# Optimization experiments

Measured on AMD Instinct MI355X. Metric: run time of the kernel, lower is better.

Reference implementation:

```python
import jax, jax.numpy as jnp
import numpy as np

N_NODES = 65536
IN_CH = 512
HIDDEN = 256          # hidden_channels[0] == encoder_hidden
OUT_CH = 8
NUM_GRAPHS = 32
MAX_LEN = 4096        # static pad bound (>= max per-graph length)
BN_EPS = 1e-5


def _make_batch_ids():
    # deterministic ragged per-graph lengths summing exactly to N_NODES
    rng = np.random.RandomState(0)
    d = rng.randint(-512, 512, size=NUM_GRAPHS)
    d[-1] -= d.sum()
    lengths = N_NODES // NUM_GRAPHS + d          # each in ~[1536, 2560] <= MAX_LEN
    return jnp.asarray(np.repeat(np.arange(NUM_GRAPHS), lengths), dtype=jnp.int32)


def setup_inputs() -> dict:
    key = jax.random.key(0)
    ks = jax.random.split(key, 12)
    f32 = jnp.float32
    inp = {
        'x_res': jax.random.normal(ks[0], (N_NODES, IN_CH), dtype=f32),
        'batch': _make_batch_ids(),
        # BatchNorm1d affine params
        'bn_gamma': jnp.ones((IN_CH,), f32),
        'bn_beta': jnp.zeros((IN_CH,), f32),
        # input2transformer: Linear(C,2H) GELU Linear(2H,H) GELU Linear(H,H)
        'W1': jax.random.normal(ks[1], (IN_CH, 2 * HIDDEN), f32) * (1.0 / np.sqrt(IN_CH)),
        'b1': jnp.zeros((2 * HIDDEN,), f32),
        'W2': jax.random.normal(ks[2], (2 * HIDDEN, HIDDEN), f32) * (1.0 / np.sqrt(2 * HIDDEN)),
        'b2': jnp.zeros((HIDDEN,), f32),
        'W3': jax.random.normal(ks[3], (HIDDEN, HIDDEN), f32) * (1.0 / np.sqrt(HIDDEN)),
        'b3': jnp.zeros((HIDDEN,), f32),
        # out_angles: Linear(encoder_hidden, out_ch) GELU DynamicTanh Tanh
        'Wo': jax.random.normal(ks[4], (HIDDEN, OUT_CH), f32) * (1.0 / np.sqrt(HIDDEN)),
        'bo': jnp.zeros((OUT_CH,), f32),
        'dyt_alpha': jnp.asarray(0.5, f32),
        'dyt_w': jnp.ones((OUT_CH,), f32),
        'dyt_b': jnp.zeros((OUT_CH,), f32),
    }
    return inp


def _forward(x_res, batch, bn_gamma, bn_beta, W1, b1, W2, b2, W3, b3,
             Wo, bo, dyt_alpha, dyt_w, dyt_b):
    # BatchNorm1d (training-mode batch stats, biased var), dropout is identity (eval)
    mu = jnp.mean(x_res, axis=0)
    var = jnp.mean((x_res - mu) ** 2, axis=0)
    x = (x_res - mu) * jax.lax.rsqrt(var + BN_EPS) * bn_gamma + bn_beta
    # input2transformer MLP (torch GELU default = exact erf)
    gelu = lambda t: jax.nn.gelu(t, approximate=False)
    x = gelu(x @ W1 + b1)
    x = gelu(x @ W2 + b2)
    x = x @ W3 + b3                                   # [N, HIDDEN]
    # ragged -> padded: scatter each node into (graph, position-in-graph)
    counts = jax.ops.segment_sum(jnp.ones_like(batch, dtype=jnp.int32), batch,
                                 num_segments=NUM_GRAPHS)
    offsets = jnp.concatenate([jnp.zeros((1,), jnp.int32),
                               jnp.cumsum(counts)[:-1].astype(jnp.int32)])
    pos = jnp.arange(N_NODES, dtype=jnp.int32) - offsets[batch]
    x_pad = jnp.zeros((NUM_GRAPHS, MAX_LEN, HIDDEN), x.dtype).at[batch, pos].set(x)
    z = jnp.transpose(x_pad, (1, 0, 2))               # [MAX_LEN, NUM_GRAPHS, HIDDEN] (stack dim=1)
    # out_angles head: Linear -> GELU -> DynamicTanh -> Tanh
    a = gelu(z @ Wo + bo)
    a = dyt_w * jnp.tanh(dyt_alpha * a) + dyt_b       # DynamicTanh (channels_last)
    return jnp.tanh(a)                                # [MAX_LEN, NUM_GRAPHS, OUT_CH]


def reference(x_res, batch, bn_gamma, bn_beta, W1, b1, W2, b2, W3, b3,
              Wo, bo, dyt_alpha, dyt_w, dyt_b):
    return _forward(x_res, batch, bn_gamma, bn_beta, W1, b1, W2, b2, W3, b3,
                    Wo, bo, dyt_alpha, dyt_w, dyt_b)
```

## Files before the change

### kernel.cpp

```cpp
#include <hip/hip_runtime.h>
#include <hip/hip_bf16.h>

#define N_NODES 65536
#define IN_CH 512
#define HIDDEN 256
#define OUT_CH 8
#define NUM_GRAPHS 32
#define MAX_LEN 4096
#define BN_EPS 1e-5f
#define BN_BLOCKS 2048

using short8  = __attribute__((ext_vector_type(8))) short;
using floatx4 = __attribute__((ext_vector_type(4))) float;
typedef unsigned int u32;
typedef unsigned short u16;

__device__ inline u16 f2b(float f) {
    u32 u = __float_as_uint(f);
    u += 0x7FFFu + ((u >> 16) & 1u);
    return (u16)(u >> 16);
}
__device__ inline float gelu_f(float x) {
    float z = x + 0.044715f * x * x * x;
    float e = __builtin_exp2f(-2.3022078f * z);
    return x * __builtin_amdgcn_rcpf(1.0f + e);
}
__device__ inline float tanh_f(float y) {
    y = fminf(fmaxf(y, -20.0f), 20.0f);
    float t = __builtin_exp2f(2.885390082f * y);
    return (t - 1.0f) * __builtin_amdgcn_rcpf(t + 1.0f);
}
__device__ inline void load_lds16(const void* g, void* l) {
    __builtin_amdgcn_global_load_lds(
        (const __attribute__((address_space(1))) u32*)g,
        (__attribute__((address_space(3))) u32*)l, 16, 0, 0);
}

__global__ __launch_bounds__(256) void statscast_k(const float* __restrict__ x,
                                                   u16* __restrict__ xb,
                                                   float4* __restrict__ partials) {
    __shared__ float4 sS[128];
    __shared__ float4 sQ[128];
    int tid = threadIdx.x;
    int half = tid >> 7;
    int c = tid & 127;
    const float4* x4 = (const float4*)x;
    uint2* xb2 = (uint2*)xb;
    float4 s = make_float4(0.f, 0.f, 0.f, 0.f);
    float4 q = make_float4(0.f, 0.f, 0.f, 0.f);
    int row0 = blockIdx.x * 32;
#pragma unroll
    for (int r = half; r < 32; r += 2) {
        size_t off = (size_t)(row0 + r) * 128 + c;
        float4 v = x4[off];
        s.x += v.x; s.y += v.y; s.z += v.z; s.w += v.w;
        q.x += v.x * v.x; q.y += v.y * v.y; q.z += v.z * v.z; q.w += v.w * v.w;
        uint2 o;
        o.x = (u32)f2b(v.x) | ((u32)f2b(v.y) << 16);
        o.y = (u32)f2b(v.z) | ((u32)f2b(v.w) << 16);
        xb2[off] = o;
    }
    if (half == 1) { sS[c] = s; sQ[c] = q; }
    __syncthreads();
    if (half == 0) {
        float4 s2 = sS[c], q2 = sQ[c];
        s.x += s2.x; s.y += s2.y; s.z += s2.z; s.w += s2.w;
        q.x += q2.x; q.y += q2.y; q.z += q2.z; q.w += q2.w;
        partials[(size_t)blockIdx.x * 256 + c * 2]     = make_float4(s.x, q.x, s.y, q.y);
        partials[(size_t)blockIdx.x * 256 + c * 2 + 1] = make_float4(s.z, q.z, s.w, q.w);
    }
}

__global__ __launch_bounds__(256) void bn_reduce_k(const float4* __restrict__ partials,
                                                   const float* __restrict__ gamma,
                                                   const float* __restrict__ beta,
                                                   float* __restrict__ scale,
                                                   float* __restrict__ shift) {
    __shared__ float4 sd[256];
    int tid = threadIdx.x;
    int g = blockIdx.x;
    float4 a = make_float4(0.f, 0.f, 0.f, 0.f);
    for (int r = tid; r < BN_BLOCKS; r += 256) {
        float4 v = partials[(size_t)r * 256 + g];
        a.x += v.x; a.y += v.y; a.z += v.z; a.w += v.w;
    }
    sd[tid] = a;
    __syncthreads();
    for (int st = 128; st > 0; st >>= 1) {
        if (tid < st) {
            float4 b = sd[tid + st];
            float4 m = sd[tid];
            m.x += b.x; m.y += b.y; m.z += b.z; m.w += b.w;
            sd[tid] = m;
        }
        __syncthreads();
    }
    if (tid == 0) {
        float4 t = sd[0];
        int c0 = g * 2, c1 = g * 2 + 1;
        const float inv = 1.0f / N_NODES;
        float mu0 = t.x * inv, var0 = t.y * inv - mu0 * mu0;
        float mu1 = t.z * inv, var1 = t.w * inv - mu1 * mu1;
        float sc0 = gamma[c0] * rsqrtf(var0 + BN_EPS);
        float sc1 = gamma[c1] * rsqrtf(var1 + BN_EPS);
        scale[c0] = sc0; shift[c0] = beta[c0] - mu0 * sc0;
        scale[c1] = sc1; shift[c1] = beta[c1] - mu1 * sc1;
    }
}

__global__ __launch_bounds__(256) void prep_k(const float* __restrict__ W1,
                                              const float* __restrict__ W2,
                                              const float* __restrict__ W3,
                                              const float* __restrict__ b1,
                                              const float* __restrict__ scale,
                                              const float* __restrict__ shift,
                                              u16* __restrict__ W1T,
                                              u16* __restrict__ W2T,
                                              u16* __restrict__ W3T,
                                              float* __restrict__ b1f,
                                              const int* __restrict__ batch,
                                              int* __restrict__ offsets) {
    int bid = blockIdx.x;
    int tid = threadIdx.x;
    if (bid < 1792) {
        int idx = bid * 256 + tid;
        if (idx < 262144) {
            int k = idx >> 9, m = idx & 511;
            W1T[(size_t)m * 512 + k] = f2b(scale[k] * W1[idx]);
        } else if (idx < 262144 + 131072) {
            int i = idx - 262144;
            int k = i >> 8, m = i & 255;
            W2T[(size_t)m * 512 + k] = f2b(W2[i]);
        } else {
            int i = idx - 393216;
            int k = i >> 8, m = i & 255;
            W3T[(size_t)m * 256 + k] = f2b(W3[i]);
        }
        if (bid == 0 && tid < NUM_GRAPHS + 1) {
            int gph = tid;
            int lo = 0, hi = N_NODES;
            while (lo < hi) {
                int mid = (lo + hi) >> 1;
                if (batch[mid] < gph) lo = mid + 1; else hi = mid;
            }
            offsets[gph] = lo;
        }
    } else {
        int m = (bid - 1792) * 256 + tid;
        float acc = b1[m];
#pragma unroll 16
        for (int k = 0; k < 512; ++k) acc += shift[k] * W1[k * 512 + m];
        b1f[m] = acc;
    }
}

template <int DO_GELU, int NXB>
__global__ __launch_bounds__(512) void gemm_bt_k(const u16* __restrict__ A,
                                                 const u16* __restrict__ BT,
                                                 const float* __restrict__ bias,
                                                 u16* __restrict__ C,
                                                 int K, int M) {
    __shared__ __align__(16) u16 As[256 * 64];
    __shared__ __align__(16) u16 Bs[128 * 64];
    int tid = threadIdx.x;
    int lane = tid & 63;
    int bid = blockIdx.x;
    int xcd = bid & 7;
    int slot = bid >> 3;
    int rloc = slot / NXB;
    int colb = slot - rloc * NXB;
    int row0 = (xcd * 32 + rloc) * 256;
    int col0 = colb * 128;
    int wave = tid >> 6;
    int wr = (wave >> 1) * 64;
    int wc = (wave & 1) * 64;
    int l15 = lane & 15;
    int q = lane >> 4;

    floatx4 acc[4][4] = {};

    const int nkt = K >> 6;
    for (int kt = 0; kt < nkt; ++kt) {
        int k0 = kt << 6;
#pragma unroll
        for (int s = 0; s < 4; ++s) {
            int li = s * 512 + tid;
            int r = li >> 3;
            int g = li & 7;
            int gs = g ^ (r & 7);
            load_lds16(&A[(size_t)(row0 + r) * K + k0 + gs * 8], &As[li * 8]);
        }
#pragma unroll
        for (int s = 0; s < 2; ++s) {
            int li = s * 512 + tid;
            int r = li >> 3;
            int g = li & 7;
            int gs = g ^ (r & 7);
            load_lds16(&BT[(size_t)(col0 + r) * K + k0 + gs * 8], &Bs[li * 8]);
        }
        __syncthreads();
#pragma unroll
        for (int ks = 0; ks < 2; ++ks) {
            int gidx = ks * 4 + q;
            short8 af[4], bg[4];
#pragma unroll
            for (int i = 0; i < 4; ++i) {
                int row = wr + i * 16 + l15;
                af[i] = *(const short8*)&As[row * 64 + (gidx ^ (row & 7)) * 8];
            }
#pragma unroll
            for (int j = 0; j < 4; ++j) {
                int row = wc + j * 16 + l15;
                bg[j] = *(const short8*)&Bs[row * 64 + (gidx ^ (row & 7)) * 8];
            }
#pragma unroll
            for (int i = 0; i < 4; ++i)
#pragma unroll
                for (int j = 0; j < 4; ++j)
                    acc[i][j] = __builtin_amdgcn_mfma_f32_16x16x32_bf16(bg[j], af[i], acc[i][j], 0, 0, 0);
        }
        __syncthreads();
    }
#pragma unroll
    for (int i = 0; i < 4; ++i) {
        size_t rbase = (size_t)(row0 + wr + i * 16 + l15) * M;
#pragma unroll
        for (int j = 0; j < 4; ++j) {
            int c = col0 + wc + j * 16 + q * 4;
            float4 b4 = *(const float4*)&bias[c];
            float v0 = acc[i][j][0] + b4.x;
            float v1 = acc[i][j][1] + b4.y;
            float v2 = acc[i][j][2] + b4.z;
            float v3 = acc[i][j][3] + b4.w;
            if (DO_GELU) { v0 = gelu_f(v0); v1 = gelu_f(v1); v2 = gelu_f(v2); v3 = gelu_f(v3); }
            uint2 pk;
            pk.x = (u32)f2b(v0) | ((u32)f2b(v1) << 16);
            pk.y = (u32)f2b(v2) | ((u32)f2b(v3) << 16);
            *(uint2*)&C[rbase + c] = pk;
        }
    }
}

__global__ __launch_bounds__(256) void head_k(const u16* __restrict__ h3,
                                              const float* __restrict__ Wo,
                                              const float* __restrict__ bo,
                                              const int* __restrict__ offsets,
                                              const float* __restrict__ alpha_p,
                                              const float* __restrict__ dyt_w,
                                              const float* __restrict__ dyt_b,
                                              float* __restrict__ out) {
    __shared__ float sWo[HIDDEN * OUT_CH];
    __shared__ int soff[NUM_GRAPHS + 1];
    int tid = threadIdx.x;
#pragma unroll
    for (int i = 0; i < 8; ++i) sWo[i * 256 + tid] = Wo[i * 256 + tid];
    if (tid < NUM_GRAPHS + 1) soff[tid] = offsets[tid];
    __syncthreads();
    int idx = blockIdx.x * 256 + tid;
    int g = idx & 31;
    int p = idx >> 5;
    int n = soff[g] + p;
    bool valid = n < soff[g + 1];
    float acc[8];
#pragma unroll
    for (int c = 0; c < 8; ++c) acc[c] = bo[c];
    if (valid) {
        const uint4* hr = (const uint4*)(h3 + (size_t)n * HIDDEN);
#pragma unroll 4
        for (int kk = 0; kk < 32; ++kk) {
            uint4 v = hr[kk];
            u32 u[4] = {v.x, v.y, v.z, v.w};
#pragma unroll
            for (int pp = 0; pp < 4; ++pp) {
                float h0 = __uint_as_float(u[pp] << 16);
                float h1 = __uint_as_float(u[pp] & 0xFFFF0000u);
                const float* w0 = &sWo[(kk * 8 + pp * 2) * 8];
                const float* w1 = w0 + 8;
#pragma unroll
                for (int c = 0; c < 8; ++c) acc[c] += h0 * w0[c];
#pragma unroll
                for (int c = 0; c < 8; ++c) acc[c] += h1 * w1[c];
            }
        }
    }
    float alpha = alpha_p[0];
    float res[8];
#pragma unroll
    for (int c = 0; c < 8; ++c) {
        float a = gelu_f(acc[c]);
        a = dyt_w[c] * tanh_f(alpha * a) + dyt_b[c];
        res[c] = tanh_f(a);
    }
    float4* o = (float4*)(out + (size_t)idx * OUT_CH);
    o[0] = make_float4(res[0], res[1], res[2], res[3]);
    o[1] = make_float4(res[4], res[5], res[6], res[7]);
}

extern "C" void kernel_launch(void* const* d_in, const int* in_sizes, int n_in,
                              void* d_out, int out_size, void* d_ws, size_t ws_size,
                              hipStream_t stream) {
    (void)in_sizes; (void)n_in; (void)out_size; (void)ws_size;
    const float* x_res = (const float*)d_in[0];
    const int*   batch = (const int*)d_in[1];
    const float* gamma = (const float*)d_in[2];
    const float* beta  = (const float*)d_in[3];
    const float* W1    = (const float*)d_in[4];
    const float* b1    = (const float*)d_in[5];
    const float* W2    = (const float*)d_in[6];
    const float* b2    = (const float*)d_in[7];
    const float* W3    = (const float*)d_in[8];
    const float* b3    = (const float*)d_in[9];
    const float* Wo    = (const float*)d_in[10];
    const float* bo    = (const float*)d_in[11];
    const float* alpha = (const float*)d_in[12];
    const float* dyt_w = (const float*)d_in[13];
    const float* dyt_b = (const float*)d_in[14];
    float* out = (float*)d_out;

    char* ws = (char*)d_ws;
    float* scale = (float*)(ws + 0);
    float* shift = (float*)(ws + 2048);
    float* b1f   = (float*)(ws + 4096);
    int*   offs  = (int*)(ws + 8192);
    u16* W1T = (u16*)(ws + 16384);
    u16* W2T = (u16*)(ws + 16384 + 524288);
    u16* W3T = (u16*)(ws + 16384 + 524288 + 262144);
    const size_t MB = 1024 * 1024;
    u16* xb = (u16*)(ws + 2 * MB);
    u16* h1 = (u16*)(ws + 66 * MB);
    u16* h2 = (u16*)(ws + 2 * MB);
    u16* h3 = (u16*)(ws + 66 * MB);
    float4* partials = (float4*)(ws + 66 * MB);

    statscast_k<<<BN_BLOCKS, 256, 0, stream>>>(x_res, xb, partials);
    bn_reduce_k<<<256, 256, 0, stream>>>(partials, gamma, beta, scale, shift);
    prep_k<<<1794, 256, 0, stream>>>(W1, W2, W3, b1, scale, shift,
                                     W1T, W2T, W3T, b1f, batch, offs);
    gemm_bt_k<1, 4><<<1024, 512, 0, stream>>>(xb, W1T, b1f, h1, 512, 512);
    gemm_bt_k<1, 2><<<512, 512, 0, stream>>>(h1, W2T, b2, h2, 512, 256);
    gemm_bt_k<0, 2><<<512, 512, 0, stream>>>(h2, W3T, b3, h3, 256, 256);
    head_k<<<512, 256, 0, stream>>>(h3, Wo, bo, offs, alpha, dyt_w, dyt_b, out);
}
```

Before: 375.6 us.

## Fuse second and third MLP GEMMs into one kernel keeping h2 in LDS

Replaces the separate W2 and W3 GEMM launches with a single kernel. Each 64-row block computes h2 = GELU(h1·W2+b2), stores it swizzled in shared memory, then multiplies it by W3 to write h3. This removes the h2 global write and read and one launch. In exchange, weight fragments are read directly from global or L2 without LDS staging, and the first GEMM is specialized with compile-time K and M.

Measured after the change: 397.2 us. 5.8% more time.

```diff
diff --git a/kernel.cpp b/kernel.cpp
--- a/kernel.cpp
+++ b/kernel.cpp
@@ -154,12 +154,11 @@
     }
 }
 
-template <int DO_GELU, int NXB>
-__global__ __launch_bounds__(512) void gemm_bt_k(const u16* __restrict__ A,
-                                                 const u16* __restrict__ BT,
-                                                 const float* __restrict__ bias,
-                                                 u16* __restrict__ C,
-                                                 int K, int M) {
+__global__ __launch_bounds__(512) void gemm1_k(const u16* __restrict__ A,
+                                               const u16* __restrict__ BT,
+                                               const float* __restrict__ bias,
+                                               u16* __restrict__ C) {
+    const int K = 512, M = 512;
     __shared__ __align__(16) u16 As[256 * 64];
     __shared__ __align__(16) u16 Bs[128 * 64];
     int tid = threadIdx.x;
@@ -167,8 +166,8 @@
     int bid = blockIdx.x;
     int xcd = bid & 7;
     int slot = bid >> 3;
-    int rloc = slot / NXB;
-    int colb = slot - rloc * NXB;
+    int rloc = slot >> 2;
+    int colb = slot & 3;
     int row0 = (xcd * 32 + rloc) * 256;
     int col0 = colb * 128;
     int wave = tid >> 6;
@@ -179,8 +178,7 @@
 
     floatx4 acc[4][4] = {};
 
-    const int nkt = K >> 6;
-    for (int kt = 0; kt < nkt; ++kt) {
+    for (int kt = 0; kt < 8; ++kt) {
         int k0 = kt << 6;
 #pragma unroll
         for (int s = 0; s < 4; ++s) {
@@ -228,15 +226,126 @@
         for (int j = 0; j < 4; ++j) {
             int c = col0 + wc + j * 16 + q * 4;
             float4 b4 = *(const float4*)&bias[c];
-            float v0 = acc[i][j][0] + b4.x;
-            float v1 = acc[i][j][1] + b4.y;
-            float v2 = acc[i][j][2] + b4.z;
-            float v3 = acc[i][j][3] + b4.w;
-            if (DO_GELU) { v0 = gelu_f(v0); v1 = gelu_f(v1); v2 = gelu_f(v2); v3 = gelu_f(v3); }
+            float v0 = gelu_f(acc[i][j][0] + b4.x);
+            float v1 = gelu_f(acc[i][j][1] + b4.y);
+            float v2 = gelu_f(acc[i][j][2] + b4.z);
+            float v3 = gelu_f(acc[i][j][3] + b4.w);
             uint2 pk;
             pk.x = (u32)f2b(v0) | ((u32)f2b(v1) << 16);
             pk.y = (u32)f2b(v2) | ((u32)f2b(v3) << 16);
             *(uint2*)&C[rbase + c] = pk;
+        }
+    }
+}
+
+__global__ __launch_bounds__(256, 3) void mlp_tail_k(const u16* __restrict__ h1,
+                                                     const u16* __restrict__ W2T,
+                                                     const u16* __restrict__ W3T,
+                                                     const float* __restrict__ b2,
+                                                     const float* __restrict__ b3,
+                                                     u16* __restrict__ h3) {
+    __shared__ __align__(16) u16 As[64 * 64];
+    __shared__ __align__(16) u16 H2[64 * 256];
+    int tid = threadIdx.x;
+    int lane = tid & 63;
+    int w = tid >> 6;
+    int l15 = lane & 15;
+    int q = lane >> 4;
+    int row0 = blockIdx.x * 64;
+
+    {
+        floatx4 acc[4][4] = {};
+        for (int kt = 0; kt < 8; ++kt) {
+            int k0 = kt << 6;
+#pragma unroll
+            for (int s = 0; s < 2; ++s) {
+                int li = s * 256 + tid;
+                int r = li >> 3;
+                int g = li & 7;
+                int gs = g ^ (r & 7);
+                load_lds16(&h1[(size_t)(row0 + r) * 512 + k0 + gs * 8], &As[li * 8]);
+            }
+            __syncthreads();
+#pragma unroll
+            for (int ks = 0; ks < 2; ++ks) {
+                int gidx = ks * 4 + q;
+                short8 af[4], bg[4];
+#pragma unroll
+                for (int j = 0; j < 4; ++j)
+                    bg[j] = *(const short8*)&W2T[(size_t)(w * 64 + j * 16 + l15) * 512 + k0 + ks * 32 + q * 8];
+#pragma unroll
+                for (int i = 0; i < 4; ++i) {
+                    int row = i * 16 + l15;
+                    af[i] = *(const short8*)&As[row * 64 + (gidx ^ (row & 7)) * 8];
+                }
+#pragma unroll
+                for (int i = 0; i < 4; ++i)
+#pragma unroll
+                    for (int j = 0; j < 4; ++j)
+                        acc[i][j] = __builtin_amdgcn_mfma_f32_16x16x32_bf16(bg[j], af[i], acc[i][j], 0, 0, 0);
+            }
+            __syncthreads();
+        }
+#pragma unroll
+        for (int j = 0; j < 4; ++j) {
+            int cl = w * 64 + j * 16 + q * 4;
+            float4 b4 = *(const float4*)&b2[cl];
+            int gg = cl >> 3;
+            int half = (q & 1) * 4;
+#pragma unroll
+            for (int i = 0; i < 4; ++i) {
+                int row = i * 16 + l15;
+                int sg = (gg & ~7) | ((gg ^ row) & 7);
+                float v0 = gelu_f(acc[i][j][0] + b4.x);
+                float v1 = gelu_f(acc[i][j][1] + b4.y);
+                float v2 = gelu_f(acc[i][j][2] + b4.z);
+                float v3 = gelu_f(acc[i][j][3] + b4.w);
+                uint2 pk;
+                pk.x = (u32)f2b(v0) | ((u32)f2b(v1) << 16);
+                pk.y = (u32)f2b(v2) | ((u32)f2b(v3) << 16);
+                *(uint2*)&H2[row * 256 + sg * 8 + half] = pk;
+            }
+        }
+    }
+    __syncthreads();
+
+    {
+        floatx4 acc[4][4] = {};
+#pragma unroll
+        for (int ks = 0; ks < 8; ++ks) {
+            int g2 = ks * 4 + q;
+            short8 af[4], bg[4];
+#pragma unroll
+            for (int j = 0; j < 4; ++j)
+                bg[j] = *(const short8*)&W3T[(size_t)(w * 64 + j * 16 + l15) * 256 + ks * 32 + q * 8];
+#pragma unroll
+            for (int i = 0; i < 4; ++i) {
+                int row = i * 16 + l15;
+                int sg = (g2 & ~7) | ((g2 ^ row) & 7);
+                af[i] = *(const short8*)&H2[row * 256 + sg * 8];
+            }
+#pragma unroll
+            for (int i = 0; i < 4; ++i)
+#pragma unroll
+                for (int j = 0; j < 4; ++j)
+                    acc[i][j] = __builtin_amdgcn_mfma_f32_16x16x32_bf16(bg[j], af[i], acc[i][j], 0, 0, 0);
+        }
+#pragma unroll
+        for (int i = 0; i < 4; ++i) {
+            size_t rbase = (size_t)(row0 + i * 16 + l15) * 256;
+#pragma unroll
+            for (int j = 0; j < 4; ++j) {
+                int c = w * 64 + j * 16 + q * 4;
+                float4 b4 = *(const float4*)&b3[c];
+                float v0 = acc[i][j][0] + b4.x;
+                float v1 = acc[i][j][1] + b4.y;
+                float v2 = acc[i][j][2] + b4.z;
+                float v3 = acc[i][j][3] + b4.w;
+                uint2 pk;
+                pk.x = (u32)f2b(v0) | ((u32)f2b(v1) << 16);
+                pk.y = (u32)f2b(v2) | ((u32)f2b(v3) << 16);
+                *(uint2*)&h3[rbase + c] = pk;
+            }
         }
     }
 }
@@ -328,16 +437,14 @@
     const size_t MB = 1024 * 1024;
     u16* xb = (u16*)(ws + 2 * MB);
     u16* h1 = (u16*)(ws + 66 * MB);
-    u16* h2 = (u16*)(ws + 2 * MB);
-    u16* h3 = (u16*)(ws + 66 * MB);
+    u16* h3 = (u16*)(ws + 2 * MB);
     float4* partials = (float4*)(ws + 66 * MB);
 
     statscast_k<<<BN_BLOCKS, 256, 0, stream>>>(x_res, xb, partials);
     bn_reduce_k<<<256, 256, 0, stream>>>(partials, gamma, beta, scale, shift);
     prep_k<<<1794, 256, 0, stream>>>(W1, W2, W3, b1, scale, shift,
                                      W1T, W2T, W3T, b1f, batch, offs);
-    gemm_bt_k<1, 4><<<1024, 512, 0, stream>>>(xb, W1T, b1f, h1, 512, 512);
-    gemm_bt_k<1, 2><<<512, 512, 0, stream>>>(h1, W2T, b2, h2, 512, 256);
-    gemm_bt_k<0, 2><<<512, 512, 0, stream>>>(h2, W3T, b3, h3, 256, 256);
+    gemm1_k<<<1024, 512, 0, stream>>>(xb, W1T, b1f, h1);
+    mlp_tail_k<<<1024, 256, 0, stream>>>(h1, W2T, W3T, b2, b3, h3);
     head_k<<<512, 256, 0, stream>>>(h3, Wo, bo, offs, alpha, dyt_w, dyt_b, out);
 }
```
